# Kernel optimization log

Hardware: AMD Instinct MI355X
Metric: run time of the kernel (lower is better)

## Reference

```python
import jax, jax.numpy as jnp
import numpy as np

NEG_INF = jnp.finfo(jnp.float32).min


def _continual_mask(attach_test_after, Q, K, test_num, chunk_size):
    """Boolean allowed-mask [B, 1, Q, K] replicating get_continual_mask +
    the per-batch test-query/train-key override in forward()."""
    k_train = K - test_num * chunk_size
    q_train = Q - test_num * chunk_size
    qi = jnp.arange(Q)[:, None]          # [Q,1]
    kj = jnp.arange(K)[None, :]          # [1,K]
    # base causal mask with diagonal offset K-Q (train queries)
    base = kj <= qi + (K - Q)            # [Q,K]
    # block-diagonal tril for test-query / test-key region
    dq = qi - q_train                    # local test row (negative for train rows, unused there)
    dk = kj - k_train
    block = (kj >= k_train) & (dk <= dq) & ((dk // chunk_size) == (dq // chunk_size))
    # per-batch: test query in chunk n may see train keys <= attach_test_after[b, n]
    chunk_idx = jnp.clip(dq[:, 0], 0, None) // chunk_size          # [Q]
    att = attach_test_after[:, chunk_idx]                          # [B,Q]
    train_key_allowed = kj[None, :, :] <= att[:, :, None]          # [B,Q,K]
    allowed = jnp.where(qi < q_train, base[None],
                        jnp.where(kj[None] < k_train, train_key_allowed, block[None]))
    return allowed[:, None]              # [B,1,Q,K]


def setup_inputs() -> dict:
    key = jax.random.key(0)
    k1, k2, k3, k4 = jax.random.split(key, 4)
    B, L, H, D = 4, 2048, 8, 64
    test_num, train_len = 64, 1536
    return {
        "queries": jax.random.normal(k1, (B, L, H, D), dtype=jnp.float32),
        "keys": jax.random.normal(k2, (B, L, H, D), dtype=jnp.float32),
        "values": jax.random.normal(k3, (B, L, H, D), dtype=jnp.float32),
        "attach_test_after": jax.random.randint(k4, (B, test_num), 0, train_len).astype(jnp.int64),
        "train_len": train_len,
    }


def reference(queries, keys, values, attach_test_after, train_len):
    B, Lq, H, Dqk = queries.shape
    test_num = attach_test_after.shape[1]
    chunk_size = (Lq - train_len) // test_num
    q = jnp.transpose(queries, (0, 2, 1, 3))   # [B,H,Lq,D]
    k = jnp.transpose(keys, (0, 2, 1, 3))      # [B,H,Lk,D]
    v = jnp.transpose(values, (0, 2, 1, 3))    # [B,H,Lk,Dv]
    Lk = k.shape[2]
    # vanilla path: scaled QK^T + continual mask + softmax + AV
    logits = jnp.einsum('bhmd,bhnd->bhmn', q, k) / jnp.sqrt(jnp.float32(Dqk))
    allowed = _continual_mask(attach_test_after, Lq, Lk, test_num, chunk_size)
    logits = jnp.where(allowed, logits, NEG_INF)
    attn = jax.nn.softmax(logits, axis=-1)
    out = jnp.einsum('bhmn,bhnd->bhmd', attn, v)
    return out.transpose(0, 2, 1, 3).reshape(B, Lq, H * v.shape[-1])  # b l (h d)
```

## Files before the change

### kernel.cpp

```cpp
#include <hip/hip_runtime.h>
#include <hip/hip_bf16.h>

typedef __bf16 bf16_t;
typedef __bf16 bf16x8 __attribute__((ext_vector_type(8)));
typedef float  f32x4  __attribute__((ext_vector_type(4)));

#define MFMA16(a, b, c) __builtin_amdgcn_mfma_f32_16x16x32_bf16((a), (b), (c), 0, 0, 0)

constexpr int Bc = 4, Lc = 2048, Hc = 8, Dc = 64;
constexpr int HD = Hc * Dc;
constexpr int TRAINc = 1536;
constexpr int ROWS_BLK = 64;
constexpr int KT = 64;

constexpr int PREPK_BLOCKS = (int)((size_t)Bc * Lc * Hc * Dc / 8 / 256);

__global__ void prep_fused(const float* __restrict__ K, bf16_t* __restrict__ Kb,
                           const float* __restrict__ V, bf16_t* __restrict__ Vt) {
  __shared__ bf16_t T[64][64];
  const int t = (int)threadIdx.x;

  if ((int)blockIdx.x < PREPK_BLOCKS) {
    size_t g = ((size_t)blockIdx.x * 256 + t) * 8;
    float4 a = *(const float4*)(K + g);
    float4 b = *(const float4*)(K + g + 4);
    bf16x8 v;
    v[0] = (bf16_t)a.x; v[1] = (bf16_t)a.y; v[2] = (bf16_t)a.z; v[3] = (bf16_t)a.w;
    v[4] = (bf16_t)b.x; v[5] = (bf16_t)b.y; v[6] = (bf16_t)b.z; v[7] = (bf16_t)b.w;
    *(bf16x8*)(Kb + g) = v;
    return;
  }

  const int bid = (int)blockIdx.x - PREPK_BLOCKS;
  const int kt = bid & 31, h = (bid >> 5) & 7, b = bid >> 8;
  {
    int kl = t >> 2, dp = (t & 3) << 4;
    const float* s = V + ((size_t)(b * Lc + kt * 64 + kl) * Hc + h) * Dc + dp;
    bf16x8 v0, v1;
    float4 f;
    f = *(const float4*)(s);      v0[0]=(bf16_t)f.x; v0[1]=(bf16_t)f.y; v0[2]=(bf16_t)f.z; v0[3]=(bf16_t)f.w;
    f = *(const float4*)(s + 4);  v0[4]=(bf16_t)f.x; v0[5]=(bf16_t)f.y; v0[6]=(bf16_t)f.z; v0[7]=(bf16_t)f.w;
    f = *(const float4*)(s + 8);  v1[0]=(bf16_t)f.x; v1[1]=(bf16_t)f.y; v1[2]=(bf16_t)f.z; v1[3]=(bf16_t)f.w;
    f = *(const float4*)(s + 12); v1[4]=(bf16_t)f.x; v1[5]=(bf16_t)f.y; v1[6]=(bf16_t)f.z; v1[7]=(bf16_t)f.w;
    const int x = kl >> 3;
    const int c0 = dp >> 3;
    *(bf16x8*)&T[kl][(c0 ^ x) << 3]       = v0;
    *(bf16x8*)&T[kl][((c0 + 1) ^ x) << 3] = v1;
  }
  __syncthreads();
  {
    int d = t >> 2, kp = (t & 3) << 4;
    const int xa = kp >> 3;
    const int xb = xa + 1;
    const int lo = d & 7, hi = d >> 3;
    const int x0 = ((hi ^ xa) << 3) + lo;
    const int x1 = ((hi ^ xb) << 3) + lo;
    bf16x8 o0, o1;
#pragma unroll
    for (int i = 0; i < 8; ++i) { o0[i] = T[kp + i][x0]; o1[i] = T[kp + 8 + i][x1]; }
    bf16_t* dst = Vt + ((size_t)((b * Hc + h) * Dc + d)) * Lc + kt * 64 + kp;
    *(bf16x8*)dst = o0;
    *(bf16x8*)(dst + 8) = o1;
  }
}

static __device__ __forceinline__ void load16(const bf16_t* g, bf16_t* l) {
  __builtin_amdgcn_global_load_lds(
      (const __attribute__((address_space(1))) unsigned int*)g,
      (__attribute__((address_space(3))) unsigned int*)l, 16, 0, 0);
}

static __device__ __forceinline__ bf16x8 mk8(unsigned w0, unsigned w1,
                                             unsigned w2, unsigned w3) {
  union { unsigned u[4]; bf16x8 v; } x;
  x.u[0] = w0; x.u[1] = w1; x.u[2] = w2; x.u[3] = w3;
  return x.v;
}

__global__ __launch_bounds__(256, 4)
void continual_attn(const float* __restrict__ Qg, const bf16_t* __restrict__ Kb,
                    const bf16_t* __restrict__ Vt, const int* __restrict__ ATT,
                    float* __restrict__ OUT)
{
  __shared__ __align__(16) bf16_t Klds[2][KT * 64];
  __shared__ __align__(16) bf16_t Vlds[2][Dc * KT];

  const int bid  = blockIdx.x;
  const int qblk = 31 - (bid >> 5);
  const int h    = bid & 7;
  const int b    = (bid >> 3) & 3;
  const int q0   = qblk * ROWS_BLK;

  const int tid  = (int)threadIdx.x;
  const int wave = tid >> 6;
  const int lane = tid & 63;
  const int quad = lane >> 4;
  const int col  = lane & 15;
  const int qw   = q0 + wave * 16;

  const size_t bhQ = (size_t)b * Lc * HD + (size_t)h * Dc;

  const int kr = tid >> 3;
  const bf16_t* ksrcA = Kb + bhQ + (size_t)kr * HD + (((tid & 7) ^ (kr & 7)) << 3);
  const bf16_t* vsrcA = Vt + ((size_t)((b * Hc + h) * Dc + kr)) * Lc + (((tid & 7) ^ (kr & 7)) << 3);
  const bf16_t* vsrcB = vsrcA + (size_t)32 * Lc;

  bf16x8 aq[2];
  {
    const float* qp = Qg + bhQ + (size_t)(qw + col) * HD + quad * 8;
    const float SC = 0.125f * 1.44269504f;
#pragma unroll
    for (int t = 0; t < 2; ++t) {
      float4 lo = *(const float4*)(qp + t * 32);
      float4 hi = *(const float4*)(qp + t * 32 + 4);
      bf16x8 v;
      v[0] = (bf16_t)(lo.x * SC); v[1] = (bf16_t)(lo.y * SC);
      v[2] = (bf16_t)(lo.z * SC); v[3] = (bf16_t)(lo.w * SC);
      v[4] = (bf16_t)(hi.x * SC); v[5] = (bf16_t)(hi.y * SC);
      v[6] = (bf16_t)(hi.z * SC); v[7] = (bf16_t)(hi.w * SC);
      aq[t] = v;
    }
  }

  const bool testblk = (q0 >= TRAINc);
  const int qi = qw + col;
  int kendL, cstartL;
  if (testblk) {
    kendL   = ATT[b * 64 + ((qi - TRAINc) >> 3)] + 1;
    cstartL = qi & ~7;
  } else {
    kendL   = qi + 1;
    cstartL = 0;
  }

  int ntA, ndiag, kfull_end;
  if (testblk) {
    int c0 = (q0 - TRAINc) >> 3;
    int amax = 0, amin = 0x7fffffff;
#pragma unroll
    for (int i = 0; i < 8; ++i) {
      int a = ATT[b * 64 + c0 + i];
      amax = (a > amax) ? a : amax;
      amin = (a < amin) ? a : amin;
    }
    ntA = (amax >> 6) + 1;
    ndiag = 1;
    kfull_end = amin + 1;
  } else {
    ntA = qblk + 1;
    ndiag = 0;
    kfull_end = q0 + 1;
  }
  const int ntot = ntA + ndiag;

  float ls[4] = {0.f, 0.f, 0.f, 0.f};
  f32x4 o[4] = {{0,0,0,0},{0,0,0,0},{0,0,0,0},{0,0,0,0}};

  const int cA = ((quad ^ (col & 7)) << 3);

  {
    bf16_t* kd = Klds[0];
    bf16_t* vd = Vlds[0];
    load16(ksrcA, kd + wave * 512);
    load16(ksrcA + (size_t)32 * HD, kd + 2048 + wave * 512);
    load16(vsrcA, vd + wave * 512);
    load16(vsrcB, vd + 2048 + wave * 512);
  }

  for (int ti = 0; ti < ntot; ++ti) {
    const int buf = ti & 1;
    __syncthreads();

    if (ti + 1 < ntot) {
      const int kn = (ti + 1 < ntA) ? (ti + 1) * KT : q0 + (ti + 1 - ntA) * KT;
      bf16_t* kd = Klds[1 - buf];
      bf16_t* vd = Vlds[1 - buf];
      load16(ksrcA + (size_t)kn * HD, kd + wave * 512);
      load16(ksrcA + (size_t)(kn + 32) * HD, kd + 2048 + wave * 512);
      load16(vsrcA + kn, vd + wave * 512);
      load16(vsrcB + kn, vd + 2048 + wave * 512);
    }

    const bf16_t* kb = Klds[buf];
    const bf16_t* vbuf = Vlds[buf];
    const int k0 = (ti < ntA) ? ti * KT : q0 + (ti - ntA) * KT;

    f32x4 sf[4] = {{0,0,0,0},{0,0,0,0},{0,0,0,0},{0,0,0,0}};
    __builtin_amdgcn_s_setprio(1);
#pragma unroll
    for (int kg = 0; kg < 4; ++kg) {
      const bf16_t* krow = kb + (kg * 16 + col) * 64;
      bf16x8 k0f = *(const bf16x8*)(krow + cA);
      bf16x8 k1f = *(const bf16x8*)(krow + (cA ^ 32));
      sf[kg] = MFMA16(k0f, aq[0], sf[kg]);
      sf[kg] = MFMA16(k1f, aq[1], sf[kg]);
    }
    __builtin_amdgcn_s_setprio(0);

    const int mode = (ti >= ntA) ? 2 : ((k0 + KT <= kfull_end) ? 0 : 1);
    if (mode == 1) {
#pragma unroll
      for (int kg = 0; kg < 4; ++kg) {
        const int kv = k0 + kg * 16 + quad * 4;
#pragma unroll
        for (int r = 0; r < 4; ++r)
          if (kv + r >= kendL) sf[kg][r] = -1e30f;
      }
    } else if (mode == 2) {
#pragma unroll
      for (int kg = 0; kg < 4; ++kg) {
        const int kv = k0 + kg * 16 + quad * 4;
#pragma unroll
        for (int r = 0; r < 4; ++r)
          if (kv + r < cstartL || kv + r > qi) sf[kg][r] = -1e30f;
      }
    }

    float pvv[4][4];
#pragma unroll
    for (int kg = 0; kg < 4; ++kg)
#pragma unroll
      for (int r = 0; r < 4; ++r) {
        float p = __builtin_amdgcn_exp2f(sf[kg][r]);
        pvv[kg][r] = p;
        ls[r] += p;
      }

    unsigned Dw[4][2];
#pragma unroll
    for (int kg = 0; kg < 4; ++kg)
#pragma unroll
      for (int d = 0; d < 2; ++d)
        asm("v_cvt_pk_bf16_f32 %0, %1, %2"
            : "=v"(Dw[kg][d]) : "v"(pvv[kg][2 * d]), "v"(pvv[kg][2 * d + 1]));

    unsigned a0 = Dw[0][0], b0 = Dw[1][0];
    asm volatile("v_permlane32_swap_b32 %0, %1" : "+v"(a0), "+v"(b0));
    asm volatile("v_permlane16_swap_b32 %0, %1" : "+v"(a0), "+v"(b0));
    unsigned a1 = Dw[0][1], b1 = Dw[1][1];
    asm volatile("v_permlane32_swap_b32 %0, %1" : "+v"(a1), "+v"(b1));
    asm volatile("v_permlane16_swap_b32 %0, %1" : "+v"(a1), "+v"(b1));
    unsigned a2 = Dw[2][0], b2 = Dw[3][0];
    asm volatile("v_permlane32_swap_b32 %0, %1" : "+v"(a2), "+v"(b2));
    asm volatile("v_permlane16_swap_b32 %0, %1" : "+v"(a2), "+v"(b2));
    unsigned a3 = Dw[2][1], b3 = Dw[3][1];
    asm volatile("v_permlane32_swap_b32 %0, %1" : "+v"(a3), "+v"(b3));
    asm volatile("v_permlane16_swap_b32 %0, %1" : "+v"(a3), "+v"(b3));

    bf16x8 pa0 = mk8(a0, a1, b0, b1);
    bf16x8 pa1 = mk8(a2, a3, b2, b3);

    __builtin_amdgcn_s_setprio(1);
#pragma unroll
    for (int t = 0; t < 4; ++t) {
      const bf16_t* vrow = vbuf + (t * 16 + col) * 64;
      bf16x8 v0 = *(const bf16x8*)(vrow + cA);
      bf16x8 v1 = *(const bf16x8*)(vrow + (cA ^ 32));
      o[t] = MFMA16(pa0, v0, o[t]);
      o[t] = MFMA16(pa1, v1, o[t]);
    }
    __builtin_amdgcn_s_setprio(0);
  }

  float rs = (ls[0] + ls[1]) + (ls[2] + ls[3]);
  rs += __shfl_xor(rs, 16);
  rs += __shfl_xor(rs, 32);
#pragma unroll
  for (int r = 0; r < 4; ++r) {
    float dr = __shfl(rs, quad * 4 + r);
    float inv = 1.f / dr;
    int qo = qw + quad * 4 + r;
    float* op = OUT + ((size_t)b * Lc + qo) * HD + (size_t)h * Dc + col;
    op[0]  = o[0][r] * inv;
    op[16] = o[1][r] * inv;
    op[32] = o[2][r] * inv;
    op[48] = o[3][r] * inv;
  }
}

extern "C" void kernel_launch(void* const* d_in, const int* in_sizes, int n_in,
                              void* d_out, int out_size, void* d_ws, size_t ws_size,
                              hipStream_t stream) {
  const float* Q   = (const float*)d_in[0];
  const float* K   = (const float*)d_in[1];
  const float* V   = (const float*)d_in[2];
  const int*   ATT = (const int*)d_in[3];
  float* OUT = (float*)d_out;
  (void)in_sizes; (void)n_in; (void)out_size; (void)ws_size;

  const size_t NE = (size_t)Bc * Lc * Hc * Dc;
  bf16_t* Kb = (bf16_t*)d_ws;
  bf16_t* Vt = Kb + NE;

  prep_fused<<<dim3((unsigned)(PREPK_BLOCKS + Bc * Hc * (Lc / 64))), dim3(256), 0, stream>>>(K, Kb, V, Vt);
  continual_attn<<<dim3(Bc * Hc * (Lc / ROWS_BLK)), dim3(256), 0, stream>>>(Q, Kb, Vt, ATT, OUT);
}
```

Before: 126.7 us.

## Switch attention kernel to 32x32 MFMA with 128-row query blocks

Replaces the 16x16x32 MFMA tiling with 32x32x16 MFMA, giving each wave 32 query rows and each block 128 rows. Every K/V tile loaded into LDS is now reused across twice as many queries, and the larger MFMA cuts instruction count and LDS reads per FLOP. The P-to-A-operand shuffle and the masking index math are rewritten for the 32x32 layout, and block scheduling interleaves heavy and light query blocks. The cost is half as many blocks (launch bounds drop to 2 blocks per CU), more registers, and coarser causal and test masking granularity, which adds wasted work on diagonal tiles.

```diff
diff --git a/kernel.cpp b/kernel.cpp
--- a/kernel.cpp
+++ b/kernel.cpp
@@ -4,13 +4,14 @@
 typedef __bf16 bf16_t;
 typedef __bf16 bf16x8 __attribute__((ext_vector_type(8)));
 typedef float  f32x4  __attribute__((ext_vector_type(4)));
-
-#define MFMA16(a, b, c) __builtin_amdgcn_mfma_f32_16x16x32_bf16((a), (b), (c), 0, 0, 0)
+typedef float  f32x16 __attribute__((ext_vector_type(16)));
+
+#define MFMA32(a, b, c) __builtin_amdgcn_mfma_f32_32x32x16_bf16((a), (b), (c), 0, 0, 0)
 
 constexpr int Bc = 4, Lc = 2048, Hc = 8, Dc = 64;
 constexpr int HD = Hc * Dc;
 constexpr int TRAINc = 1536;
-constexpr int ROWS_BLK = 64;
+constexpr int ROWS_BLK = 128;
 constexpr int KT = 64;
 
 constexpr int PREPK_BLOCKS = (int)((size_t)Bc * Lc * Hc * Dc / 8 / 256);
@@ -77,7 +78,7 @@
   return x.v;
 }
 
-__global__ __launch_bounds__(256, 4)
+__global__ __launch_bounds__(256, 2)
 void continual_attn(const float* __restrict__ Qg, const bf16_t* __restrict__ Kb,
                     const bf16_t* __restrict__ Vt, const int* __restrict__ ATT,
                     float* __restrict__ OUT)
@@ -86,7 +87,8 @@
   __shared__ __align__(16) bf16_t Vlds[2][Dc * KT];
 
   const int bid  = blockIdx.x;
-  const int qblk = 31 - (bid >> 5);
+  const int g    = bid >> 5;
+  const int qblk = (g < 8) ? (15 - g) : (g - 8);
   const int h    = bid & 7;
   const int b    = (bid >> 3) & 3;
   const int q0   = qblk * ROWS_BLK;
@@ -94,9 +96,10 @@
   const int tid  = (int)threadIdx.x;
   const int wave = tid >> 6;
   const int lane = tid & 63;
-  const int quad = lane >> 4;
-  const int col  = lane & 15;
-  const int qw   = q0 + wave * 16;
+  const int hi   = lane >> 5;
+  const int lq   = lane & 31;
+  const int qw   = q0 + wave * 32;
+  const int qi   = qw + lq;
 
   const size_t bhQ = (size_t)b * Lc * HD + (size_t)h * Dc;
 
@@ -105,25 +108,24 @@
   const bf16_t* vsrcA = Vt + ((size_t)((b * Hc + h) * Dc + kr)) * Lc + (((tid & 7) ^ (kr & 7)) << 3);
   const bf16_t* vsrcB = vsrcA + (size_t)32 * Lc;
 
-  bf16x8 aq[2];
-  {
-    const float* qp = Qg + bhQ + (size_t)(qw + col) * HD + quad * 8;
+  bf16x8 bq[4];
+  {
+    const float* qp = Qg + bhQ + (size_t)qi * HD + 8 * hi;
     const float SC = 0.125f * 1.44269504f;
 #pragma unroll
-    for (int t = 0; t < 2; ++t) {
-      float4 lo = *(const float4*)(qp + t * 32);
-      float4 hi = *(const float4*)(qp + t * 32 + 4);
+    for (int s = 0; s < 4; ++s) {
+      float4 lo = *(const float4*)(qp + 16 * s);
+      float4 h4 = *(const float4*)(qp + 16 * s + 4);
       bf16x8 v;
       v[0] = (bf16_t)(lo.x * SC); v[1] = (bf16_t)(lo.y * SC);
       v[2] = (bf16_t)(lo.z * SC); v[3] = (bf16_t)(lo.w * SC);
-      v[4] = (bf16_t)(hi.x * SC); v[5] = (bf16_t)(hi.y * SC);
-      v[6] = (bf16_t)(hi.z * SC); v[7] = (bf16_t)(hi.w * SC);
-      aq[t] = v;
+      v[4] = (bf16_t)(h4.x * SC); v[5] = (bf16_t)(h4.y * SC);
+      v[6] = (bf16_t)(h4.z * SC); v[7] = (bf16_t)(h4.w * SC);
+      bq[s] = v;
     }
   }
 
   const bool testblk = (q0 >= TRAINc);
-  const int qi = qw + col;
   int kendL, cstartL;
   if (testblk) {
     kendL   = ATT[b * 64 + ((qi - TRAINc) >> 3)] + 1;
@@ -138,33 +140,32 @@
     int c0 = (q0 - TRAINc) >> 3;
     int amax = 0, amin = 0x7fffffff;
 #pragma unroll
-    for (int i = 0; i < 8; ++i) {
+    for (int i = 0; i < 16; ++i) {
       int a = ATT[b * 64 + c0 + i];
       amax = (a > amax) ? a : amax;
       amin = (a < amin) ? a : amin;
     }
     ntA = (amax >> 6) + 1;
-    ndiag = 1;
+    ndiag = 2;
     kfull_end = amin + 1;
   } else {
-    ntA = qblk + 1;
+    ntA = 2 * qblk + 2;
     ndiag = 0;
     kfull_end = q0 + 1;
   }
   const int ntot = ntA + ndiag;
 
   float ls[4] = {0.f, 0.f, 0.f, 0.f};
-  f32x4 o[4] = {{0,0,0,0},{0,0,0,0},{0,0,0,0},{0,0,0,0}};
-
-  const int cA = ((quad ^ (col & 7)) << 3);
-
-  {
-    bf16_t* kd = Klds[0];
-    bf16_t* vd = Vlds[0];
-    load16(ksrcA, kd + wave * 512);
-    load16(ksrcA + (size_t)32 * HD, kd + 2048 + wave * 512);
-    load16(vsrcA, vd + wave * 512);
-    load16(vsrcB, vd + 2048 + wave * 512);
+  f32x16 o0 = {0,0,0,0,0,0,0,0,0,0,0,0,0,0,0,0};
+  f32x16 o1 = {0,0,0,0,0,0,0,0,0,0,0,0,0,0,0,0};
+
+  const int swz = lq & 7;
+
+  {
+    load16(ksrcA, Klds[0] + wave * 512);
+    load16(ksrcA + (size_t)32 * HD, Klds[0] + 2048 + wave * 512);
+    load16(vsrcA, Vlds[0] + wave * 512);
+    load16(vsrcB, Vlds[0] + 2048 + wave * 512);
   }
 
   for (int ti = 0; ti < ntot; ++ti) {
@@ -185,96 +186,86 @@
     const bf16_t* vbuf = Vlds[buf];
     const int k0 = (ti < ntA) ? ti * KT : q0 + (ti - ntA) * KT;
 
-    f32x4 sf[4] = {{0,0,0,0},{0,0,0,0},{0,0,0,0},{0,0,0,0}};
+    f32x16 s0 = {0,0,0,0,0,0,0,0,0,0,0,0,0,0,0,0};
+    f32x16 s1 = {0,0,0,0,0,0,0,0,0,0,0,0,0,0,0,0};
     __builtin_amdgcn_s_setprio(1);
 #pragma unroll
-    for (int kg = 0; kg < 4; ++kg) {
-      const bf16_t* krow = kb + (kg * 16 + col) * 64;
-      bf16x8 k0f = *(const bf16x8*)(krow + cA);
-      bf16x8 k1f = *(const bf16x8*)(krow + (cA ^ 32));
-      sf[kg] = MFMA16(k0f, aq[0], sf[kg]);
-      sf[kg] = MFMA16(k1f, aq[1], sf[kg]);
+    for (int s = 0; s < 4; ++s) {
+      const int sl = ((2 * s + hi) ^ swz) << 3;
+      bf16x8 ka0 = *(const bf16x8*)(kb + lq * 64 + sl);
+      bf16x8 ka1 = *(const bf16x8*)(kb + (lq + 32) * 64 + sl);
+      s0 = MFMA32(ka0, bq[s], s0);
+      s1 = MFMA32(ka1, bq[s], s1);
     }
     __builtin_amdgcn_s_setprio(0);
 
     const int mode = (ti >= ntA) ? 2 : ((k0 + KT <= kfull_end) ? 0 : 1);
     if (mode == 1) {
 #pragma unroll
-      for (int kg = 0; kg < 4; ++kg) {
-        const int kv = k0 + kg * 16 + quad * 4;
-#pragma unroll
-        for (int r = 0; r < 4; ++r)
-          if (kv + r >= kendL) sf[kg][r] = -1e30f;
+      for (int c = 0; c < 16; ++c) {
+        const int kv = k0 + (c & 3) + 8 * (c >> 2) + 4 * hi;
+        if (kv >= kendL)      s0[c] = -1e30f;
+        if (kv + 32 >= kendL) s1[c] = -1e30f;
       }
     } else if (mode == 2) {
 #pragma unroll
-      for (int kg = 0; kg < 4; ++kg) {
-        const int kv = k0 + kg * 16 + quad * 4;
-#pragma unroll
-        for (int r = 0; r < 4; ++r)
-          if (kv + r < cstartL || kv + r > qi) sf[kg][r] = -1e30f;
+      for (int c = 0; c < 16; ++c) {
+        const int kv = k0 + (c & 3) + 8 * (c >> 2) + 4 * hi;
+        if (kv < cstartL || kv > qi)           s0[c] = -1e30f;
+        if (kv + 32 < cstartL || kv + 32 > qi) s1[c] = -1e30f;
       }
     }
 
-    float pvv[4][4];
-#pragma unroll
-    for (int kg = 0; kg < 4; ++kg)
-#pragma unroll
-      for (int r = 0; r < 4; ++r) {
-        float p = __builtin_amdgcn_exp2f(sf[kg][r]);
-        pvv[kg][r] = p;
-        ls[r] += p;
-      }
-
-    unsigned Dw[4][2];
-#pragma unroll
-    for (int kg = 0; kg < 4; ++kg)
-#pragma unroll
-      for (int d = 0; d < 2; ++d)
-        asm("v_cvt_pk_bf16_f32 %0, %1, %2"
-            : "=v"(Dw[kg][d]) : "v"(pvv[kg][2 * d]), "v"(pvv[kg][2 * d + 1]));
-
-    unsigned a0 = Dw[0][0], b0 = Dw[1][0];
-    asm volatile("v_permlane32_swap_b32 %0, %1" : "+v"(a0), "+v"(b0));
-    asm volatile("v_permlane16_swap_b32 %0, %1" : "+v"(a0), "+v"(b0));
-    unsigned a1 = Dw[0][1], b1 = Dw[1][1];
-    asm volatile("v_permlane32_swap_b32 %0, %1" : "+v"(a1), "+v"(b1));
-    asm volatile("v_permlane16_swap_b32 %0, %1" : "+v"(a1), "+v"(b1));
-    unsigned a2 = Dw[2][0], b2 = Dw[3][0];
-    asm volatile("v_permlane32_swap_b32 %0, %1" : "+v"(a2), "+v"(b2));
-    asm volatile("v_permlane16_swap_b32 %0, %1" : "+v"(a2), "+v"(b2));
-    unsigned a3 = Dw[2][1], b3 = Dw[3][1];
-    asm volatile("v_permlane32_swap_b32 %0, %1" : "+v"(a3), "+v"(b3));
-    asm volatile("v_permlane16_swap_b32 %0, %1" : "+v"(a3), "+v"(b3));
-
-    bf16x8 pa0 = mk8(a0, a1, b0, b1);
-    bf16x8 pa1 = mk8(a2, a3, b2, b3);
+    float p0[16], p1[16];
+#pragma unroll
+    for (int c = 0; c < 16; ++c) {
+      p0[c] = __builtin_amdgcn_exp2f(s0[c]);
+      p1[c] = __builtin_amdgcn_exp2f(s1[c]);
+      ls[c & 3] += p0[c] + p1[c];
+    }
+
+    unsigned D0[8], D1[8];
+#pragma unroll
+    for (int j = 0; j < 8; ++j) {
+      asm("v_cvt_pk_bf16_f32 %0, %1, %2" : "=v"(D0[j]) : "v"(p0[2*j]), "v"(p0[2*j+1]));
+      asm("v_cvt_pk_bf16_f32 %0, %1, %2" : "=v"(D1[j]) : "v"(p1[2*j]), "v"(p1[2*j+1]));
+    }
+#pragma unroll
+    for (int j = 0; j < 2; ++j) {
+      asm volatile("v_permlane32_swap_b32 %0, %1" : "+v"(D0[4*j]),   "+v"(D0[4*j+2]));
+      asm volatile("v_permlane32_swap_b32 %0, %1" : "+v"(D0[4*j+1]), "+v"(D0[4*j+3]));
+      asm volatile("v_permlane32_swap_b32 %0, %1" : "+v"(D1[4*j]),   "+v"(D1[4*j+2]));
+      asm volatile("v_permlane32_swap_b32 %0, %1" : "+v"(D1[4*j+1]), "+v"(D1[4*j+3]));
+    }
+    bf16x8 pA[4];
+    pA[0] = mk8(D0[0], D0[1], D0[2], D0[3]);
+    pA[1] = mk8(D0[4], D0[5], D0[6], D0[7]);
+    pA[2] = mk8(D1[0], D1[1], D1[2], D1[3]);
+    pA[3] = mk8(D1[4], D1[5], D1[6], D1[7]);
 
     __builtin_amdgcn_s_setprio(1);
 #pragma unroll
     for (int t = 0; t < 4; ++t) {
-      const bf16_t* vrow = vbuf + (t * 16 + col) * 64;
-      bf16x8 v0 = *(const bf16x8*)(vrow + cA);
-      bf16x8 v1 = *(const bf16x8*)(vrow + (cA ^ 32));
-      o[t] = MFMA16(pa0, v0, o[t]);
-      o[t] = MFMA16(pa1, v1, o[t]);
+      const int sl = ((2 * t + hi) ^ swz) << 3;
+      bf16x8 v0 = *(const bf16x8*)(vbuf + lq * 64 + sl);
+      bf16x8 v1 = *(const bf16x8*)(vbuf + (lq + 32) * 64 + sl);
+      o0 = MFMA32(pA[t], v0, o0);
+      o1 = MFMA32(pA[t], v1, o1);
     }
     __builtin_amdgcn_s_setprio(0);
   }
 
   float rs = (ls[0] + ls[1]) + (ls[2] + ls[3]);
-  rs += __shfl_xor(rs, 16);
   rs += __shfl_xor(rs, 32);
-#pragma unroll
-  for (int r = 0; r < 4; ++r) {
-    float dr = __shfl(rs, quad * 4 + r);
+
+#pragma unroll
+  for (int c = 0; c < 16; ++c) {
+    const int qlocal = (c & 3) + 8 * (c >> 2) + 4 * hi;
+    float dr = __shfl(rs, qlocal);
     float inv = 1.f / dr;
-    int qo = qw + quad * 4 + r;
-    float* op = OUT + ((size_t)b * Lc + qo) * HD + (size_t)h * Dc + col;
-    op[0]  = o[0][r] * inv;
-    op[16] = o[1][r] * inv;
-    op[32] = o[2][r] * inv;
-    op[48] = o[3][r] * inv;
+    float* op = OUT + ((size_t)b * Lc + (qw + qlocal)) * HD + (size_t)h * Dc + lq;
+    op[0]  = o0[c] * inv;
+    op[32] = o1[c] * inv;
   }
 }
 
```

Result: slower. 133.1 us (+5.1%).

## Fuse K/V bf16 conversion and V transpose into attention kernel, drop prep pass

Applied to the files above, without the earlier changes.

Removes the separate prep kernel that converted K to bf16 and transposed V through a workspace. The attention kernel now loads fp32 K/V tiles into registers two tiles ahead, converts and writes them swizzled into LDS itself, and moves the barrier to the end of each iteration. Block ordering also changes so the test-query blocks (qblk 24-31) are scheduled first. This saves a kernel launch and a workspace round trip, but every block re-reads and re-converts fp32 K/V with strided scalar V loads, which raises register pressure and global traffic.

```diff
diff --git a/kernel.cpp b/kernel.cpp
--- a/kernel.cpp
+++ b/kernel.cpp
@@ -13,80 +13,17 @@
 constexpr int ROWS_BLK = 64;
 constexpr int KT = 64;
 
-constexpr int PREPK_BLOCKS = (int)((size_t)Bc * Lc * Hc * Dc / 8 / 256);
-
-__global__ void prep_fused(const float* __restrict__ K, bf16_t* __restrict__ Kb,
-                           const float* __restrict__ V, bf16_t* __restrict__ Vt) {
-  __shared__ bf16_t T[64][64];
-  const int t = (int)threadIdx.x;
-
-  if ((int)blockIdx.x < PREPK_BLOCKS) {
-    size_t g = ((size_t)blockIdx.x * 256 + t) * 8;
-    float4 a = *(const float4*)(K + g);
-    float4 b = *(const float4*)(K + g + 4);
-    bf16x8 v;
-    v[0] = (bf16_t)a.x; v[1] = (bf16_t)a.y; v[2] = (bf16_t)a.z; v[3] = (bf16_t)a.w;
-    v[4] = (bf16_t)b.x; v[5] = (bf16_t)b.y; v[6] = (bf16_t)b.z; v[7] = (bf16_t)b.w;
-    *(bf16x8*)(Kb + g) = v;
-    return;
-  }
-
-  const int bid = (int)blockIdx.x - PREPK_BLOCKS;
-  const int kt = bid & 31, h = (bid >> 5) & 7, b = bid >> 8;
-  {
-    int kl = t >> 2, dp = (t & 3) << 4;
-    const float* s = V + ((size_t)(b * Lc + kt * 64 + kl) * Hc + h) * Dc + dp;
-    bf16x8 v0, v1;
-    float4 f;
-    f = *(const float4*)(s);      v0[0]=(bf16_t)f.x; v0[1]=(bf16_t)f.y; v0[2]=(bf16_t)f.z; v0[3]=(bf16_t)f.w;
-    f = *(const float4*)(s + 4);  v0[4]=(bf16_t)f.x; v0[5]=(bf16_t)f.y; v0[6]=(bf16_t)f.z; v0[7]=(bf16_t)f.w;
-    f = *(const float4*)(s + 8);  v1[0]=(bf16_t)f.x; v1[1]=(bf16_t)f.y; v1[2]=(bf16_t)f.z; v1[3]=(bf16_t)f.w;
-    f = *(const float4*)(s + 12); v1[4]=(bf16_t)f.x; v1[5]=(bf16_t)f.y; v1[6]=(bf16_t)f.z; v1[7]=(bf16_t)f.w;
-    const int x = kl >> 3;
-    const int c0 = dp >> 3;
-    *(bf16x8*)&T[kl][(c0 ^ x) << 3]       = v0;
-    *(bf16x8*)&T[kl][((c0 + 1) ^ x) << 3] = v1;
-  }
-  __syncthreads();
-  {
-    int d = t >> 2, kp = (t & 3) << 4;
-    const int xa = kp >> 3;
-    const int xb = xa + 1;
-    const int lo = d & 7, hi = d >> 3;
-    const int x0 = ((hi ^ xa) << 3) + lo;
-    const int x1 = ((hi ^ xb) << 3) + lo;
-    bf16x8 o0, o1;
-#pragma unroll
-    for (int i = 0; i < 8; ++i) { o0[i] = T[kp + i][x0]; o1[i] = T[kp + 8 + i][x1]; }
-    bf16_t* dst = Vt + ((size_t)((b * Hc + h) * Dc + d)) * Lc + kt * 64 + kp;
-    *(bf16x8*)dst = o0;
-    *(bf16x8*)(dst + 8) = o1;
-  }
-}
-
-static __device__ __forceinline__ void load16(const bf16_t* g, bf16_t* l) {
-  __builtin_amdgcn_global_load_lds(
-      (const __attribute__((address_space(1))) unsigned int*)g,
-      (__attribute__((address_space(3))) unsigned int*)l, 16, 0, 0);
-}
-
-static __device__ __forceinline__ bf16x8 mk8(unsigned w0, unsigned w1,
-                                             unsigned w2, unsigned w3) {
-  union { unsigned u[4]; bf16x8 v; } x;
-  x.u[0] = w0; x.u[1] = w1; x.u[2] = w2; x.u[3] = w3;
-  return x.v;
-}
-
 __global__ __launch_bounds__(256, 4)
-void continual_attn(const float* __restrict__ Qg, const bf16_t* __restrict__ Kb,
-                    const bf16_t* __restrict__ Vt, const int* __restrict__ ATT,
+void continual_attn(const float* __restrict__ Qg, const float* __restrict__ Kf,
+                    const float* __restrict__ Vf, const int* __restrict__ ATT,
                     float* __restrict__ OUT)
 {
   __shared__ __align__(16) bf16_t Klds[2][KT * 64];
   __shared__ __align__(16) bf16_t Vlds[2][Dc * KT];
 
   const int bid  = blockIdx.x;
-  const int qblk = 31 - (bid >> 5);
+  const int g    = bid >> 5;
+  const int qblk = (g < 8) ? (24 + g) : (31 - g);
   const int h    = bid & 7;
   const int b    = (bid >> 3) & 3;
   const int q0   = qblk * ROWS_BLK;
@@ -100,10 +37,47 @@
 
   const size_t bhQ = (size_t)b * Lc * HD + (size_t)h * Dc;
 
-  const int kr = tid >> 3;
-  const bf16_t* ksrcA = Kb + bhQ + (size_t)kr * HD + (((tid & 7) ^ (kr & 7)) << 3);
-  const bf16_t* vsrcA = Vt + ((size_t)((b * Hc + h) * Dc + kr)) * Lc + (((tid & 7) ^ (kr & 7)) << 3);
-  const bf16_t* vsrcB = vsrcA + (size_t)32 * Lc;
+  const float* ksrcF = Kf + bhQ + (size_t)(tid >> 2) * HD + (tid & 3) * 16;
+  const float* vsrcF = Vf + bhQ + (tid & 63);
+  const int    vgk   = 16 * (tid >> 6);
+
+  float kst[16], vst[16];
+
+  auto LOADT = [&](int k0v) {
+#pragma unroll
+    for (int i = 0; i < 4; ++i)
+      *(float4*)(kst + 4 * i) = *(const float4*)(ksrcF + (size_t)k0v * HD + 4 * i);
+#pragma unroll
+    for (int j = 0; j < 16; ++j)
+      vst[j] = vsrcF[(size_t)(k0v + vgk + j) * HD];
+  };
+
+  auto mk8l = [](unsigned w0, unsigned w1, unsigned w2, unsigned w3) {
+    union { unsigned u[4]; bf16x8 v; } x;
+    x.u[0] = w0; x.u[1] = w1; x.u[2] = w2; x.u[3] = w3;
+    return x.v;
+  };
+
+  auto CVTW = [&](int bi) {
+    unsigned kd[8], vd[8];
+#pragma unroll
+    for (int m = 0; m < 8; ++m) {
+      asm("v_cvt_pk_bf16_f32 %0, %1, %2" : "=v"(kd[m]) : "v"(kst[2*m]), "v"(kst[2*m+1]));
+      asm("v_cvt_pk_bf16_f32 %0, %1, %2" : "=v"(vd[m]) : "v"(vst[2*m]), "v"(vst[2*m+1]));
+    }
+    {
+      const int r = tid >> 2, cb = 2 * (tid & 3);
+      bf16_t* kt = Klds[bi] + r * 64;
+      *(bf16x8*)(kt + (((cb    ) ^ (r & 7)) << 3)) = mk8l(kd[0], kd[1], kd[2], kd[3]);
+      *(bf16x8*)(kt + (((cb + 1) ^ (r & 7)) << 3)) = mk8l(kd[4], kd[5], kd[6], kd[7]);
+    }
+    {
+      const int d = tid & 63, g2 = 2 * (tid >> 6);
+      bf16_t* vt = Vlds[bi] + d * 64;
+      *(bf16x8*)(vt + (((g2    ) ^ (d & 7)) << 3)) = mk8l(vd[0], vd[1], vd[2], vd[3]);
+      *(bf16x8*)(vt + (((g2 + 1) ^ (d & 7)) << 3)) = mk8l(vd[4], vd[5], vd[6], vd[7]);
+    }
+  };
 
   bf16x8 aq[2];
   {
@@ -153,37 +127,25 @@
   }
   const int ntot = ntA + ndiag;
 
+  auto tk = [&](int t) { return (t < ntA) ? t * KT : q0 + (t - ntA) * KT; };
+
   float ls[4] = {0.f, 0.f, 0.f, 0.f};
   f32x4 o[4] = {{0,0,0,0},{0,0,0,0},{0,0,0,0},{0,0,0,0}};
 
   const int cA = ((quad ^ (col & 7)) << 3);
 
-  {
-    bf16_t* kd = Klds[0];
-    bf16_t* vd = Vlds[0];
-    load16(ksrcA, kd + wave * 512);
-    load16(ksrcA + (size_t)32 * HD, kd + 2048 + wave * 512);
-    load16(vsrcA, vd + wave * 512);
-    load16(vsrcB, vd + 2048 + wave * 512);
-  }
+  LOADT(0);
+  CVTW(0);
+  if (ntot > 1) LOADT(tk(1));
+  __syncthreads();
 
   for (int ti = 0; ti < ntot; ++ti) {
-    const int buf = ti & 1;
-    __syncthreads();
-
-    if (ti + 1 < ntot) {
-      const int kn = (ti + 1 < ntA) ? (ti + 1) * KT : q0 + (ti + 1 - ntA) * KT;
-      bf16_t* kd = Klds[1 - buf];
-      bf16_t* vd = Vlds[1 - buf];
-      load16(ksrcA + (size_t)kn * HD, kd + wave * 512);
-      load16(ksrcA + (size_t)(kn + 32) * HD, kd + 2048 + wave * 512);
-      load16(vsrcA + kn, vd + wave * 512);
-      load16(vsrcB + kn, vd + 2048 + wave * 512);
-    }
-
-    const bf16_t* kb = Klds[buf];
-    const bf16_t* vbuf = Vlds[buf];
-    const int k0 = (ti < ntA) ? ti * KT : q0 + (ti - ntA) * KT;
+    if (ti + 1 < ntot) CVTW((ti + 1) & 1);
+    if (ti + 2 < ntot) LOADT(tk(ti + 2));
+
+    const bf16_t* kb   = Klds[ti & 1];
+    const bf16_t* vbuf = Vlds[ti & 1];
+    const int k0 = tk(ti);
 
     f32x4 sf[4] = {{0,0,0,0},{0,0,0,0},{0,0,0,0},{0,0,0,0}};
     __builtin_amdgcn_s_setprio(1);
@@ -247,8 +209,8 @@
     asm volatile("v_permlane32_swap_b32 %0, %1" : "+v"(a3), "+v"(b3));
     asm volatile("v_permlane16_swap_b32 %0, %1" : "+v"(a3), "+v"(b3));
 
-    bf16x8 pa0 = mk8(a0, a1, b0, b1);
-    bf16x8 pa1 = mk8(a2, a3, b2, b3);
+    bf16x8 pa0 = mk8l(a0, a1, b0, b1);
+    bf16x8 pa1 = mk8l(a2, a3, b2, b3);
 
     __builtin_amdgcn_s_setprio(1);
 #pragma unroll
@@ -260,6 +222,8 @@
       o[t] = MFMA16(pa1, v1, o[t]);
     }
     __builtin_amdgcn_s_setprio(0);
+
+    __syncthreads();
   }
 
   float rs = (ls[0] + ls[1]) + (ls[2] + ls[3]);
@@ -286,12 +250,7 @@
   const float* V   = (const float*)d_in[2];
   const int*   ATT = (const int*)d_in[3];
   float* OUT = (float*)d_out;
-  (void)in_sizes; (void)n_in; (void)out_size; (void)ws_size;
-
-  const size_t NE = (size_t)Bc * Lc * Hc * Dc;
-  bf16_t* Kb = (bf16_t*)d_ws;
-  bf16_t* Vt = Kb + NE;
-
-  prep_fused<<<dim3((unsigned)(PREPK_BLOCKS + Bc * Hc * (Lc / 64))), dim3(256), 0, stream>>>(K, Kb, V, Vt);
-  continual_attn<<<dim3(Bc * Hc * (Lc / ROWS_BLK)), dim3(256), 0, stream>>>(Q, Kb, Vt, ATT, OUT);
+  (void)in_sizes; (void)n_in; (void)out_size; (void)d_ws; (void)ws_size;
+
+  continual_attn<<<dim3(Bc * Hc * (Lc / ROWS_BLK)), dim3(256), 0, stream>>>(Q, K, V, ATT, OUT);
 }
```

New measurement: 123.6 us. 1.02x faster.
